# Kernel tuning notes

Measured on AMD Instinct MI355X. Metric: run time of the kernel, lower is better.

## Reference

```python
import jax, jax.numpy as jnp
from jax import lax
import numpy as np

TOP_K = 2
CAPACITY_FACTOR = 1.0


def setup_inputs() -> dict:
    key = jax.random.key(0)
    kx, kg, k1, k2 = jax.random.split(key, 4)
    B, S, D, F, E = 8, 4096, 512, 1024, 16
    x = jax.random.normal(kx, (B, S, D), dtype=jnp.float32)
    w_gate = jax.random.normal(kg, (D, E), dtype=jnp.float32) * 0.02
    w1 = jax.random.normal(k1, (E, D, 2 * F), dtype=jnp.float32) * 0.02
    w2 = jax.random.normal(k2, (E, F, D), dtype=jnp.float32) * 0.02
    return {"x": x, "w_gate": w_gate, "w1": w1, "w2": w2}


def reference(x, w_gate, w1, w2):
    # Inference mode: no gating noise, dropout is identity.
    B, S, D = x.shape
    E = w_gate.shape[1]
    T = B * S
    capacity = max(1, int(CAPACITY_FACTOR * T / E))  # static

    flat = x.reshape(T, D)
    gate_logits = flat @ w_gate                      # [T, E]
    gate_scores = jax.nn.softmax(gate_logits, axis=-1)
    topk_vals, topk_idx = lax.top_k(gate_scores, TOP_K)  # [T, k]

    phi_mean = gate_scores.mean(axis=0)
    aux_loss = E * jnp.sum(phi_mean * phi_mean)

    # Per-expert combine weight for every token: [E, T]
    onehot = topk_idx[None, :, :] == jnp.arange(E)[:, None, None]  # [E, T, k]
    w_et = jnp.sum(jnp.where(onehot, topk_vals[None], 0.0), axis=-1)  # [E, T]

    # Capacity truncation: keep the `capacity` highest-weight tokens per expert
    sel_w, sel_idx = lax.top_k(w_et, capacity)  # [E, C]; unrouted picks have weight 0

    xs = flat[sel_idx]                                  # [E, C, D] gather
    h = jnp.einsum('ecd,edf->ecf', xs, w1)              # [E, C, 2F]
    h1, h2 = jnp.split(h, 2, axis=-1)
    act = h1 * jax.nn.silu(h2)                          # SwiGLU
    out_e = jnp.einsum('ecf,efd->ecd', act, w2) * sel_w[..., None]  # [E, C, D]

    combined = jnp.zeros((T, D), dtype=flat.dtype).at[sel_idx.reshape(-1)].add(
        out_e.reshape(-1, D))
    return combined.reshape(B, S, D), aux_loss
```

## Files before the change

kernel.cpp:

```cpp
#include <hip/hip_runtime.h>
#include <hip/hip_bf16.h>
#include <math.h>

#define T_TOK 32768
#define D_DIM 512
#define E_EXP 16
#define F_DIM 1024
#define C_CAP 2048

typedef __attribute__((ext_vector_type(8))) __bf16 bf16x8;
typedef __attribute__((ext_vector_type(4))) float f32x4;

__device__ __forceinline__ unsigned short f2bf(float f) {
  unsigned u = __float_as_uint(f);
  u += 0x7FFFu + ((u >> 16) & 1u);
  return (unsigned short)(u >> 16);
}

__device__ __forceinline__ void gld16(const void* gptr, void* ldsptr) {
  __builtin_amdgcn_global_load_lds(
      (__attribute__((address_space(1))) void*)(void*)gptr,
      (__attribute__((address_space(3))) void*)ldsptr, 16, 0, 0);
}

__global__ void transpose_conv_kernel(const float* __restrict__ in,
                                      unsigned short* __restrict__ out,
                                      int R, int Cc) {
  __shared__ float tile[32][33];
  int e = blockIdx.z;
  int r0 = blockIdx.y * 32, c0 = blockIdx.x * 32;
  const float* pin = in + (size_t)e * R * Cc;
  unsigned short* pout = out + (size_t)e * R * Cc;
  int tx = threadIdx.x, ty = threadIdx.y;
  #pragma unroll
  for (int i = 0; i < 32; i += 8)
    tile[ty + i][tx] = pin[(size_t)(r0 + ty + i) * Cc + c0 + tx];
  __syncthreads();
  #pragma unroll
  for (int i = 0; i < 32; i += 8)
    pout[(size_t)(c0 + ty + i) * R + r0 + tx] = f2bf(tile[tx][ty + i]);
}

__global__ __launch_bounds__(256) void gate_kernel(
    const float* __restrict__ x, const float* __restrict__ wg,
    float* __restrict__ w_et, float* __restrict__ phi_sum,
    unsigned short* __restrict__ xb) {
  __shared__ float wgl[D_DIM * E_EXP];
  __shared__ float phil[E_EXP];
  int tid = threadIdx.x;
  for (int i = tid; i < D_DIM * E_EXP; i += 256) wgl[i] = wg[i];
  if (tid < E_EXP) phil[tid] = 0.f;
  __syncthreads();

  int g = tid >> 4;
  int e = tid & 15;
  int t = blockIdx.x * 16 + g;

  float acc = 0.f;
  const float* xr = x + (size_t)t * D_DIM;
  #pragma unroll 4
  for (int d = 0; d < D_DIM; d += 4) {
    float4 xv = *(const float4*)(xr + d);
    acc = fmaf(xv.x, wgl[(d + 0) * 16 + e], acc);
    acc = fmaf(xv.y, wgl[(d + 1) * 16 + e], acc);
    acc = fmaf(xv.z, wgl[(d + 2) * 16 + e], acc);
    acc = fmaf(xv.w, wgl[(d + 3) * 16 + e], acc);
  }

  unsigned short* xrow = xb + (size_t)t * D_DIM;
  #pragma unroll
  for (int j = 0; j < 8; ++j) {
    int idx = j * 16 + e;
    float4 v = *(const float4*)(xr + idx * 4);
    ushort4 o;
    o.x = f2bf(v.x); o.y = f2bf(v.y); o.z = f2bf(v.z); o.w = f2bf(v.w);
    ((ushort4*)xrow)[idx] = o;
  }

  float m = acc;
  for (int off = 8; off; off >>= 1) m = fmaxf(m, __shfl_xor(m, off));
  float p = expf(acc - m);
  float s = p;
  for (int off = 8; off; off >>= 1) s += __shfl_xor(s, off);
  float score = p / s;
  atomicAdd(&phil[e], score);

  float v1 = score; int i1 = e;
  for (int off = 8; off; off >>= 1) {
    float ov = __shfl_xor(v1, off); int oi = __shfl_xor(i1, off);
    if (ov > v1 || (ov == v1 && oi < i1)) { v1 = ov; i1 = oi; }
  }
  float sc2 = (e == i1) ? -1.f : score;
  float v2 = sc2; int i2 = e;
  for (int off = 8; off; off >>= 1) {
    float ov = __shfl_xor(v2, off); int oi = __shfl_xor(i2, off);
    if (ov > v2 || (ov == v2 && oi < i2)) { v2 = ov; i2 = oi; }
  }
  if (e == 0) {
    w_et[(size_t)i1 * T_TOK + t] = v1;
    w_et[(size_t)i2 * T_TOK + t] = v2;
  }
  __syncthreads();
  if (tid < E_EXP) atomicAdd(&phi_sum[tid], phil[tid]);
}

__global__ void aux_kernel(const float* __restrict__ phi_sum, float* __restrict__ out_aux) {
  if (threadIdx.x == 0) {
    float s = 0.f;
    for (int e = 0; e < E_EXP; ++e) {
      float pm = phi_sum[e] / (float)T_TOK;
      s += pm * pm;
    }
    *out_aux = (float)E_EXP * s;
  }
}

__global__ __launch_bounds__(1024) void select_kernel(
    const float* __restrict__ w_et, int* __restrict__ sel_idx, float* __restrict__ sel_w) {
  int e = blockIdx.x, tid = threadIdx.x;
  const float* w = w_et + (size_t)e * T_TOK;
  __shared__ unsigned hist[256];
  __shared__ unsigned scan_buf[1024];
  __shared__ unsigned sh_prefix, sh_k, sh_ngt, sh_cnt;

  unsigned prefix = 0, k = C_CAP, n_gt = 0;
  for (int pass = 0; pass < 4; ++pass) {
    int shift = 24 - pass * 8;
    if (tid < 256) hist[tid] = 0;
    if (tid == 0) sh_cnt = 0;
    __syncthreads();
    for (int i = tid; i < T_TOK; i += 1024) {
      unsigned b = __float_as_uint(w[i]);
      bool match = (pass == 0) || ((b >> (shift + 8)) == (prefix >> (shift + 8)));
      if (match) atomicAdd(&hist[(b >> shift) & 0xFFu], 1u);
    }
    __syncthreads();
    if (tid == 0) {
      unsigned cum = 0; int b = 255;
      for (; b > 0; --b) {
        unsigned c = hist[b];
        if (cum + c >= k) break;
        cum += c;
      }
      sh_prefix = prefix | ((unsigned)b << shift);
      sh_k = k - cum;
      sh_ngt = n_gt + cum;
    }
    __syncthreads();
    prefix = sh_prefix; k = sh_k; n_gt = sh_ngt;
    __syncthreads();
  }

  unsigned thr = prefix;
  unsigned eq_take = k;
  int base = tid * 32;

  unsigned myeq = 0;
  for (int i = base; i < base + 32; ++i) {
    float v = w[i];
    unsigned b = __float_as_uint(v);
    if (b > thr) {
      unsigned pos = atomicAdd(&sh_cnt, 1u);
      sel_idx[(size_t)e * C_CAP + pos] = i;
      sel_w[(size_t)e * C_CAP + pos] = v;
    } else if (b == thr) {
      myeq++;
    }
  }
  scan_buf[tid] = myeq;
  __syncthreads();
  for (int off = 1; off < 1024; off <<= 1) {
    unsigned add = (tid >= off) ? scan_buf[tid - off] : 0u;
    __syncthreads();
    scan_buf[tid] += add;
    __syncthreads();
  }
  unsigned excl = scan_buf[tid] - myeq;

  if (thr != 0u) {
    unsigned r = excl;
    for (int i = base; i < base + 32 && r < eq_take; ++i) {
      unsigned b = __float_as_uint(w[i]);
      if (b == thr) {
        sel_idx[(size_t)e * C_CAP + n_gt + r] = i;
        sel_w[(size_t)e * C_CAP + n_gt + r] = w[i];
        r++;
      }
    }
  }
  unsigned m_e = (thr != 0u) ? (unsigned)C_CAP : n_gt;
  for (unsigned i = m_e + tid; i < C_CAP; i += 1024) {
    sel_idx[(size_t)e * C_CAP + i] = 0;
    sel_w[(size_t)e * C_CAP + i] = 0.f;
  }
}

__global__ __launch_bounds__(256) void gemm1_kernel(
    const unsigned short* __restrict__ xb,
    const unsigned short* __restrict__ w1t,
    const int* __restrict__ sel_idx,
    unsigned short* __restrict__ act) {
  __shared__ __align__(16) unsigned short As[128 * 64];
  __shared__ __align__(16) unsigned short Bs[128 * 64];
  int bid = (blockIdx.x & 7) * 512 + (blockIdx.x >> 3);
  int nt = bid & 15, mt = (bid >> 4) & 15, e = bid >> 8;
  int tid = threadIdx.x, lane = tid & 63, wid = tid >> 6;

  const unsigned short* ag[4];
  const unsigned short* bg[4];
  unsigned lofs[4];
  #pragma unroll
  for (int s = 0; s < 4; ++s) {
    int c = s * 256 + tid;
    int row = c >> 3, kc = c & 7;
    int kcs = kc ^ (row & 7);
    int tok = sel_idx[e * C_CAP + mt * 128 + row];
    ag[s] = xb + (size_t)tok * D_DIM + kcs * 8;
    int hcol = (row < 64) ? (nt * 64 + row) : (F_DIM + nt * 64 + (row - 64));
    bg[s] = w1t + ((size_t)e * 2 * F_DIM + hcol) * D_DIM + kcs * 8;
    lofs[s] = (unsigned)(s * 256 + wid * 64) * 16;
  }

  f32x4 zero = {0.f, 0.f, 0.f, 0.f};
  f32x4 acc[2][8];
  #pragma unroll
  for (int m = 0; m < 2; ++m)
    #pragma unroll
    for (int n = 0; n < 8; ++n) acc[m][n] = zero;

  int cl = lane & 15, rg = lane >> 4;
  int sw = cl & 7;

  for (int kt = 0; kt < D_DIM / 64; ++kt) {
    #pragma unroll
    for (int s = 0; s < 4; ++s) {
      gld16(ag[s] + kt * 64, (char*)As + lofs[s]);
      gld16(bg[s] + kt * 64, (char*)Bs + lofs[s]);
    }
    __syncthreads();
    #pragma unroll
    for (int kk = 0; kk < 64; kk += 32) {
      int cofs = (((kk >> 3) + rg) ^ sw) << 3;
      bf16x8 a[2], b[8];
      #pragma unroll
      for (int m = 0; m < 2; ++m)
        a[m] = *(const bf16x8*)&As[(wid * 32 + m * 16 + cl) * 64 + cofs];
      #pragma unroll
      for (int n = 0; n < 8; ++n)
        b[n] = *(const bf16x8*)&Bs[(n * 16 + cl) * 64 + cofs];
      #pragma unroll
      for (int m = 0; m < 2; ++m)
        #pragma unroll
        for (int n = 0; n < 8; ++n)
          acc[m][n] = __builtin_amdgcn_mfma_f32_16x16x32_bf16(a[m], b[n], acc[m][n], 0, 0, 0);
    }
    __syncthreads();
  }

  #pragma unroll
  for (int m = 0; m < 2; ++m) {
    #pragma unroll
    for (int n = 0; n < 4; ++n) {
      #pragma unroll
      for (int r = 0; r < 4; ++r) {
        int row = mt * 128 + wid * 32 + m * 16 + rg * 4 + r;
        int col = nt * 64 + n * 16 + cl;
        float h1 = acc[m][n][r];
        float h2 = acc[m][n + 4][r];
        float sg = h2 / (1.f + __expf(-h2));
        act[((size_t)e * C_CAP + row) * F_DIM + col] = f2bf(h1 * sg);
      }
    }
  }
}

__global__ __launch_bounds__(256) void gemm2_kernel(
    const unsigned short* __restrict__ act,
    const unsigned short* __restrict__ w2t,
    const int* __restrict__ sel_idx,
    const float* __restrict__ sel_w,
    float* __restrict__ out) {
  __shared__ __align__(16) unsigned short As[128 * 64];
  __shared__ __align__(16) unsigned short Bs[128 * 64];
  int bid = (blockIdx.x & 7) * 128 + (blockIdx.x >> 3);
  int nt = bid & 3, mt = (bid >> 2) & 15, e = bid >> 6;
  int tid = threadIdx.x, lane = tid & 63, wid = tid >> 6;
  int wr = wid >> 1, wc = wid & 1;

  const unsigned short* ag[4];
  const unsigned short* bg[4];
  unsigned lofs[4];
  #pragma unroll
  for (int s = 0; s < 4; ++s) {
    int c = s * 256 + tid;
    int row = c >> 3, kc = c & 7;
    int kcs = kc ^ (row & 7);
    ag[s] = act + ((size_t)e * C_CAP + mt * 128 + row) * F_DIM + kcs * 8;
    int dcol = nt * 128 + row;
    bg[s] = w2t + ((size_t)e * D_DIM + dcol) * F_DIM + kcs * 8;
    lofs[s] = (unsigned)(s * 256 + wid * 64) * 16;
  }

  f32x4 zero = {0.f, 0.f, 0.f, 0.f};
  f32x4 acc[4][4];
  #pragma unroll
  for (int m = 0; m < 4; ++m)
    #pragma unroll
    for (int n = 0; n < 4; ++n) acc[m][n] = zero;

  int cl = lane & 15, rg = lane >> 4;
  int sw = cl & 7;

  for (int kt = 0; kt < F_DIM / 64; ++kt) {
    #pragma unroll
    for (int s = 0; s < 4; ++s) {
      gld16(ag[s] + kt * 64, (char*)As + lofs[s]);
      gld16(bg[s] + kt * 64, (char*)Bs + lofs[s]);
    }
    __syncthreads();
    #pragma unroll
    for (int kk = 0; kk < 64; kk += 32) {
      int cofs = (((kk >> 3) + rg) ^ sw) << 3;
      bf16x8 a[4], b[4];
      #pragma unroll
      for (int m = 0; m < 4; ++m)
        a[m] = *(const bf16x8*)&As[(wr * 64 + m * 16 + cl) * 64 + cofs];
      #pragma unroll
      for (int n = 0; n < 4; ++n)
        b[n] = *(const bf16x8*)&Bs[(wc * 64 + n * 16 + cl) * 64 + cofs];
      #pragma unroll
      for (int m = 0; m < 4; ++m)
        #pragma unroll
        for (int n = 0; n < 4; ++n)
          acc[m][n] = __builtin_amdgcn_mfma_f32_16x16x32_bf16(a[m], b[n], acc[m][n], 0, 0, 0);
    }
    __syncthreads();
  }

  #pragma unroll
  for (int m = 0; m < 4; ++m) {
    #pragma unroll
    for (int r = 0; r < 4; ++r) {
      int slot = mt * 128 + wr * 64 + m * 16 + rg * 4 + r;
      float wgt = sel_w[e * C_CAP + slot];
      int tok = sel_idx[e * C_CAP + slot];
      float* orow = out + (size_t)tok * D_DIM;
      #pragma unroll
      for (int n = 0; n < 4; ++n) {
        int col = nt * 128 + wc * 64 + n * 16 + cl;
        atomicAdd(&orow[col], acc[m][n][r] * wgt);
      }
    }
  }
}

extern "C" void kernel_launch(void* const* d_in, const int* in_sizes, int n_in,
                              void* d_out, int out_size, void* d_ws, size_t ws_size,
                              hipStream_t stream) {
  const float* x  = (const float*)d_in[0];
  const float* wg = (const float*)d_in[1];
  const float* w1 = (const float*)d_in[2];
  const float* w2 = (const float*)d_in[3];
  float* out = (float*)d_out;

  char* ws = (char*)d_ws;
  size_t off = 0;
  auto carve = [&](size_t bytes) -> void* {
    void* p = ws + off;
    off += (bytes + 255) & ~(size_t)255;
    return p;
  };
  float* w_et            = (float*)carve((size_t)E_EXP * T_TOK * 4);
  float* phi             = (float*)carve(64);
  int* sel_i             = (int*)carve((size_t)E_EXP * C_CAP * 4);
  float* sel_wv          = (float*)carve((size_t)E_EXP * C_CAP * 4);
  unsigned short* xb     = (unsigned short*)carve((size_t)T_TOK * D_DIM * 2);
  unsigned short* w1t    = (unsigned short*)carve((size_t)E_EXP * 2 * F_DIM * D_DIM * 2);
  unsigned short* w2t    = (unsigned short*)carve((size_t)E_EXP * D_DIM * F_DIM * 2);
  unsigned short* actb   = (unsigned short*)carve((size_t)E_EXP * C_CAP * F_DIM * 2);
  if (off > ws_size) return;

  hipMemsetAsync(w_et, 0, (size_t)E_EXP * T_TOK * 4, stream);
  hipMemsetAsync(phi, 0, 64, stream);
  hipMemsetAsync(d_out, 0, (size_t)out_size * 4, stream);

  transpose_conv_kernel<<<dim3(2 * F_DIM / 32, D_DIM / 32, E_EXP), dim3(32, 8), 0, stream>>>(
      w1, w1t, D_DIM, 2 * F_DIM);
  transpose_conv_kernel<<<dim3(D_DIM / 32, F_DIM / 32, E_EXP), dim3(32, 8), 0, stream>>>(
      w2, w2t, F_DIM, D_DIM);
  gate_kernel<<<T_TOK / 16, 256, 0, stream>>>(x, wg, w_et, phi, xb);
  select_kernel<<<E_EXP, 1024, 0, stream>>>(w_et, sel_i, sel_wv);
  aux_kernel<<<1, 64, 0, stream>>>(phi, out + (size_t)T_TOK * D_DIM);
  gemm1_kernel<<<E_EXP * 16 * 16, 256, 0, stream>>>(xb, w1t, sel_i, actb);
  gemm2_kernel<<<E_EXP * 16 * 4, 256, 0, stream>>>(actb, w2t, sel_i, sel_wv, out);
}
```

Baseline: 410.6 us.

## Parallelize capacity top-k selection and triple-buffer both expert GEMMs

The single-block-per-expert radix select is replaced by a multi-kernel, grid-parallel radix select over 11/11/10-bit digits, followed by count, prefix-base and write phases spread across 256 blocks. Both GEMM kernels move to a BK=32, three-stage LDS pipeline using async global-to-LDS loads with explicit vmcnt waits, plus a new swizzle and a 2x2 wave tiling for gemm1. The aim is to remove the serial bottleneck of 16 blocks scanning 32K elements and to hide global load latency in the GEMMs. The cost is more kernel launches and extra histogram buffers that must be zeroed, and the select path now handles the case of fewer than capacity nonzero weights differently.

Result: faster. 336.4 us (-18.1%).

```diff
diff --git a/kernel.cpp b/kernel.cpp
--- a/kernel.cpp
+++ b/kernel.cpp
@@ -115,191 +115,283 @@
   }
 }
 
-__global__ __launch_bounds__(1024) void select_kernel(
-    const float* __restrict__ w_et, int* __restrict__ sel_idx, float* __restrict__ sel_w) {
-  int e = blockIdx.x, tid = threadIdx.x;
-  const float* w = w_et + (size_t)e * T_TOK;
-  __shared__ unsigned hist[256];
-  __shared__ unsigned scan_buf[1024];
-  __shared__ unsigned sh_prefix, sh_k, sh_ngt, sh_cnt;
-
-  unsigned prefix = 0, k = C_CAP, n_gt = 0;
-  for (int pass = 0; pass < 4; ++pass) {
-    int shift = 24 - pass * 8;
-    if (tid < 256) hist[tid] = 0;
-    if (tid == 0) sh_cnt = 0;
+template<int P>
+__global__ __launch_bounds__(256) void s_hist(
+    const float* __restrict__ w_et, unsigned* __restrict__ hist,
+    const unsigned* __restrict__ prefix, const unsigned* __restrict__ done) {
+  int c = blockIdx.x, e = blockIdx.y, tid = threadIdx.x;
+  if (P > 0 && done[e]) return;
+  __shared__ unsigned lh[2048];
+  for (int i = tid; i < 2048; i += 256) lh[i] = 0;
+  __syncthreads();
+  const float* w = w_et + (size_t)e * T_TOK + c * 2048;
+  unsigned pfx = (P > 0) ? prefix[e] : 0u;
+  #pragma unroll
+  for (int i = 0; i < 8; ++i) {
+    unsigned b = __float_as_uint(w[i * 256 + tid]);
+    if (P == 0) { if (b) atomicAdd(&lh[b >> 21], 1u); }
+    else if (P == 1) { if ((b >> 21) == (pfx >> 21)) atomicAdd(&lh[(b >> 10) & 0x7FFu], 1u); }
+    else { if ((b >> 10) == (pfx >> 10)) atomicAdd(&lh[b & 0x3FFu], 1u); }
+  }
+  __syncthreads();
+  for (int i = tid; i < 2048; i += 256)
+    if (lh[i]) atomicAdd(&hist[e * 2048 + i], lh[i]);
+}
+
+template<int P>
+__global__ __launch_bounds__(1024) void s_pick(
+    const unsigned* __restrict__ hist, unsigned* __restrict__ prefix,
+    unsigned* __restrict__ krem, unsigned* __restrict__ done) {
+  int tid = threadIdx.x, lane = tid & 63, e = tid >> 6;
+  if (P > 0 && done[e]) return;
+  const int BPL = (P == 2) ? 16 : 32;
+  const int SH = (P == 0) ? 21 : (P == 1) ? 10 : 0;
+  const unsigned* h = hist + e * 2048;
+  unsigned S = 0;
+  for (int i = 0; i < BPL; ++i) S += h[lane * BPL + i];
+  unsigned U = S;
+  #pragma unroll
+  for (int off = 1; off < 64; off <<= 1) {
+    unsigned t = __shfl_down(U, off);
+    if (lane + off < 64) U += t;
+  }
+  unsigned Unext = __shfl_down(U, 1);
+  if (lane == 63) Unext = 0;
+  unsigned k = (P == 0) ? (unsigned)C_CAP : krem[e];
+  if (P == 0 && lane == 0) {
+    if (U < k) { done[e] = 1; prefix[e] = 0; krem[e] = 0; }
+    else done[e] = 0;
+  }
+  if (U >= k && Unext < k) {
+    unsigned cum = Unext; int chosen = 0; unsigned knew = 0;
+    for (int i = BPL - 1; i >= 0; --i) {
+      unsigned hh = h[lane * BPL + i];
+      if (cum + hh >= k) { chosen = lane * BPL + i; knew = k - cum; break; }
+      cum += hh;
+    }
+    if (P == 0) prefix[e] = ((unsigned)chosen) << SH;
+    else prefix[e] = prefix[e] | (((unsigned)chosen) << SH);
+    krem[e] = knew;
+  }
+}
+
+__global__ __launch_bounds__(256) void s_count(
+    const float* __restrict__ w_et, const unsigned* __restrict__ prefix,
+    unsigned* __restrict__ cnt) {
+  int c = blockIdx.x, e = blockIdx.y, tid = threadIdx.x;
+  unsigned thr = prefix[e];
+  const uint4* up = (const uint4*)(w_et + (size_t)e * T_TOK + c * 2048 + tid * 8);
+  uint4 va = up[0], vb = up[1];
+  unsigned gt = 0, eq = 0;
+  unsigned vals[8] = {va.x, va.y, va.z, va.w, vb.x, vb.y, vb.z, vb.w};
+  #pragma unroll
+  for (int i = 0; i < 8; ++i) {
+    if (vals[i] > thr) gt++;
+    else if (vals[i] == thr) eq++;
+  }
+  __shared__ unsigned sc[256];
+  sc[tid] = (gt << 16) | eq;
+  __syncthreads();
+  for (int s = 128; s; s >>= 1) {
+    if (tid < s) sc[tid] += sc[tid + s];
     __syncthreads();
-    for (int i = tid; i < T_TOK; i += 1024) {
-      unsigned b = __float_as_uint(w[i]);
-      bool match = (pass == 0) || ((b >> (shift + 8)) == (prefix >> (shift + 8)));
-      if (match) atomicAdd(&hist[(b >> shift) & 0xFFu], 1u);
+  }
+  if (tid == 0) cnt[e * 16 + c] = sc[0];
+}
+
+__global__ __launch_bounds__(64) void s_base(
+    const unsigned* __restrict__ cnt, unsigned* __restrict__ gbase,
+    unsigned* __restrict__ ebase, unsigned* __restrict__ gtt,
+    unsigned* __restrict__ eqt) {
+  int e = threadIdx.x;
+  if (e >= 16) return;
+  unsigned g = 0, q = 0;
+  #pragma unroll
+  for (int c = 0; c < 16; ++c) {
+    unsigned p = cnt[e * 16 + c];
+    gbase[e * 16 + c] = g;
+    ebase[e * 16 + c] = q;
+    g += p >> 16;
+    q += p & 0xFFFFu;
+  }
+  gtt[e] = g;
+  eqt[e] = (unsigned)C_CAP - g;
+}
+
+__global__ __launch_bounds__(256) void s_write(
+    const float* __restrict__ w_et, const unsigned* __restrict__ prefix,
+    const unsigned* __restrict__ gbase, const unsigned* __restrict__ ebase,
+    const unsigned* __restrict__ gtt, const unsigned* __restrict__ eqt,
+    int* __restrict__ sel_idx, float* __restrict__ sel_w) {
+  int c = blockIdx.x, e = blockIdx.y, tid = threadIdx.x;
+  unsigned thr = prefix[e];
+  const uint4* up = (const uint4*)(w_et + (size_t)e * T_TOK + c * 2048 + tid * 8);
+  uint4 va = up[0], vb = up[1];
+  unsigned vals[8] = {va.x, va.y, va.z, va.w, vb.x, vb.y, vb.z, vb.w};
+  unsigned gt = 0, eq = 0;
+  #pragma unroll
+  for (int i = 0; i < 8; ++i) {
+    if (vals[i] > thr) gt++;
+    else if (vals[i] == thr) eq++;
+  }
+  __shared__ unsigned sc[256];
+  unsigned mine = (gt << 16) | eq;
+  sc[tid] = mine;
+  __syncthreads();
+  for (int off = 1; off < 256; off <<= 1) {
+    unsigned add = (tid >= off) ? sc[tid - off] : 0u;
+    __syncthreads();
+    sc[tid] += add;
+    __syncthreads();
+  }
+  unsigned excl = sc[tid] - mine;
+  unsigned gpos = gbase[e * 16 + c] + (excl >> 16);
+  unsigned qpos = ebase[e * 16 + c] + (excl & 0xFFFFu);
+  unsigned gtotal = gtt[e], eqtake = eqt[e];
+  int* si = sel_idx + (size_t)e * C_CAP;
+  float* sw = sel_w + (size_t)e * C_CAP;
+  int tokbase = c * 2048 + tid * 8;
+  #pragma unroll
+  for (int i = 0; i < 8; ++i) {
+    unsigned b = vals[i];
+    if (b > thr) {
+      si[gpos] = tokbase + i; sw[gpos] = __uint_as_float(b); gpos++;
+    } else if (b == thr && qpos < eqtake) {
+      si[gtotal + qpos] = tokbase + i; sw[gtotal + qpos] = __uint_as_float(b); qpos++;
     }
-    __syncthreads();
-    if (tid == 0) {
-      unsigned cum = 0; int b = 255;
-      for (; b > 0; --b) {
-        unsigned c = hist[b];
-        if (cum + c >= k) break;
-        cum += c;
-      }
-      sh_prefix = prefix | ((unsigned)b << shift);
-      sh_k = k - cum;
-      sh_ngt = n_gt + cum;
-    }
-    __syncthreads();
-    prefix = sh_prefix; k = sh_k; n_gt = sh_ngt;
-    __syncthreads();
-  }
-
-  unsigned thr = prefix;
-  unsigned eq_take = k;
-  int base = tid * 32;
-
-  unsigned myeq = 0;
-  for (int i = base; i < base + 32; ++i) {
-    float v = w[i];
-    unsigned b = __float_as_uint(v);
-    if (b > thr) {
-      unsigned pos = atomicAdd(&sh_cnt, 1u);
-      sel_idx[(size_t)e * C_CAP + pos] = i;
-      sel_w[(size_t)e * C_CAP + pos] = v;
-    } else if (b == thr) {
-      myeq++;
-    }
-  }
-  scan_buf[tid] = myeq;
-  __syncthreads();
-  for (int off = 1; off < 1024; off <<= 1) {
-    unsigned add = (tid >= off) ? scan_buf[tid - off] : 0u;
-    __syncthreads();
-    scan_buf[tid] += add;
-    __syncthreads();
-  }
-  unsigned excl = scan_buf[tid] - myeq;
-
-  if (thr != 0u) {
-    unsigned r = excl;
-    for (int i = base; i < base + 32 && r < eq_take; ++i) {
-      unsigned b = __float_as_uint(w[i]);
-      if (b == thr) {
-        sel_idx[(size_t)e * C_CAP + n_gt + r] = i;
-        sel_w[(size_t)e * C_CAP + n_gt + r] = w[i];
-        r++;
-      }
-    }
-  }
-  unsigned m_e = (thr != 0u) ? (unsigned)C_CAP : n_gt;
-  for (unsigned i = m_e + tid; i < C_CAP; i += 1024) {
-    sel_idx[(size_t)e * C_CAP + i] = 0;
-    sel_w[(size_t)e * C_CAP + i] = 0.f;
-  }
-}
-
-__global__ __launch_bounds__(256) void gemm1_kernel(
+  }
+}
+
+
+#define PIPE_BARRIER() do { __builtin_amdgcn_s_barrier(); __builtin_amdgcn_sched_barrier(0); } while (0)
+
+__global__ __launch_bounds__(256, 3) void gemm1_kernel(
     const unsigned short* __restrict__ xb,
     const unsigned short* __restrict__ w1t,
     const int* __restrict__ sel_idx,
     unsigned short* __restrict__ act) {
-  __shared__ __align__(16) unsigned short As[128 * 64];
-  __shared__ __align__(16) unsigned short Bs[128 * 64];
+  __shared__ __align__(16) unsigned short As[3 * 4096];
+  __shared__ __align__(16) unsigned short Bs[3 * 4096];
   int bid = (blockIdx.x & 7) * 512 + (blockIdx.x >> 3);
   int nt = bid & 15, mt = (bid >> 4) & 15, e = bid >> 8;
   int tid = threadIdx.x, lane = tid & 63, wid = tid >> 6;
-
-  const unsigned short* ag[4];
-  const unsigned short* bg[4];
-  unsigned lofs[4];
-  #pragma unroll
-  for (int s = 0; s < 4; ++s) {
-    int c = s * 256 + tid;
-    int row = c >> 3, kc = c & 7;
-    int kcs = kc ^ (row & 7);
-    int tok = sel_idx[e * C_CAP + mt * 128 + row];
-    ag[s] = xb + (size_t)tok * D_DIM + kcs * 8;
-    int hcol = (row < 64) ? (nt * 64 + row) : (F_DIM + nt * 64 + (row - 64));
-    bg[s] = w1t + ((size_t)e * 2 * F_DIM + hcol) * D_DIM + kcs * 8;
-    lofs[s] = (unsigned)(s * 256 + wid * 64) * 16;
-  }
+  int wr = wid >> 1, wc = wid & 1;
+  int cl = lane & 15, rg = lane >> 4;
+
+  int c0 = tid, c1 = 256 + tid;
+  int r0 = c0 >> 2, gk0 = (c0 & 3) ^ ((r0 >> 1) & 3);
+  int r1 = c1 >> 2, gk1 = (c1 & 3) ^ ((r1 >> 1) & 3);
+  int tok0 = sel_idx[e * C_CAP + mt * 128 + r0];
+  int tok1 = sel_idx[e * C_CAP + mt * 128 + r1];
+  const unsigned short* ag0 = xb + (size_t)tok0 * D_DIM + gk0 * 8;
+  const unsigned short* ag1 = xb + (size_t)tok1 * D_DIM + gk1 * 8;
+  int hcol0 = (r0 < 64) ? (nt * 64 + r0) : (F_DIM + nt * 64 + (r0 - 64));
+  int hcol1 = (r1 < 64) ? (nt * 64 + r1) : (F_DIM + nt * 64 + (r1 - 64));
+  const unsigned short* bg0 = w1t + ((size_t)e * 2 * F_DIM + hcol0) * D_DIM + gk0 * 8;
+  const unsigned short* bg1 = w1t + ((size_t)e * 2 * F_DIM + hcol1) * D_DIM + gk1 * 8;
+  char* Ab = (char*)As;
+  char* Bb = (char*)Bs;
+
+#define G1_STAGE(buf, kt) do { \
+    gld16(ag0 + (kt) * 32, Ab + (buf) * 8192 + tid * 16); \
+    gld16(ag1 + (kt) * 32, Ab + (buf) * 8192 + 4096 + tid * 16); \
+    gld16(bg0 + (kt) * 32, Bb + (buf) * 8192 + tid * 16); \
+    gld16(bg1 + (kt) * 32, Bb + (buf) * 8192 + 4096 + tid * 16); \
+  } while (0)
 
   f32x4 zero = {0.f, 0.f, 0.f, 0.f};
-  f32x4 acc[2][8];
-  #pragma unroll
-  for (int m = 0; m < 2; ++m)
+  f32x4 acc[4][4];
+  #pragma unroll
+  for (int m = 0; m < 4; ++m)
     #pragma unroll
-    for (int n = 0; n < 8; ++n) acc[m][n] = zero;
-
-  int cl = lane & 15, rg = lane >> 4;
-  int sw = cl & 7;
-
-  for (int kt = 0; kt < D_DIM / 64; ++kt) {
+    for (int n = 0; n < 4; ++n) acc[m][n] = zero;
+
+#define G1_COMPUTE(buf) do { \
+    const unsigned short* Ap = As + (buf) * 4096; \
+    const unsigned short* Bp = Bs + (buf) * 4096; \
+    bf16x8 av[4], bv[4]; \
+    _Pragma("unroll") \
+    for (int m = 0; m < 4; ++m) { \
+      int ra = wr * 64 + m * 16 + cl; \
+      av[m] = *(const bf16x8*)&Ap[(ra * 4 + (rg ^ ((ra >> 1) & 3))) * 8]; \
+    } \
+    _Pragma("unroll") \
+    for (int n = 0; n < 4; ++n) { \
+      int rb = ((n < 2) ? (wc * 32 + n * 16) : (64 + wc * 32 + (n - 2) * 16)) + cl; \
+      bv[n] = *(const bf16x8*)&Bp[(rb * 4 + (rg ^ ((rb >> 1) & 3))) * 8]; \
+    } \
+    _Pragma("unroll") \
+    for (int m = 0; m < 4; ++m) \
+      _Pragma("unroll") \
+      for (int n = 0; n < 4; ++n) \
+        acc[m][n] = __builtin_amdgcn_mfma_f32_16x16x32_bf16(av[m], bv[n], acc[m][n], 0, 0, 0); \
+  } while (0)
+
+  const int NK = D_DIM / 32;
+  G1_STAGE(0, 0);
+  G1_STAGE(1, 1);
+  int bc = 0, bs = 2;
+  for (int kt = 0; kt < NK - 1; ++kt) {
+    asm volatile("s_waitcnt vmcnt(4)" ::: "memory");
+    PIPE_BARRIER();
+    if (kt + 2 < NK) { G1_STAGE(bs, kt + 2); bs = (bs == 2) ? 0 : bs + 1; }
+    __builtin_amdgcn_sched_barrier(0);
+    G1_COMPUTE(bc);
+    bc = (bc == 2) ? 0 : bc + 1;
+  }
+  asm volatile("s_waitcnt vmcnt(0)" ::: "memory");
+  PIPE_BARRIER();
+  G1_COMPUTE(bc);
+
+  #pragma unroll
+  for (int m = 0; m < 4; ++m) {
     #pragma unroll
-    for (int s = 0; s < 4; ++s) {
-      gld16(ag[s] + kt * 64, (char*)As + lofs[s]);
-      gld16(bg[s] + kt * 64, (char*)Bs + lofs[s]);
-    }
-    __syncthreads();
-    #pragma unroll
-    for (int kk = 0; kk < 64; kk += 32) {
-      int cofs = (((kk >> 3) + rg) ^ sw) << 3;
-      bf16x8 a[2], b[8];
-      #pragma unroll
-      for (int m = 0; m < 2; ++m)
-        a[m] = *(const bf16x8*)&As[(wid * 32 + m * 16 + cl) * 64 + cofs];
-      #pragma unroll
-      for (int n = 0; n < 8; ++n)
-        b[n] = *(const bf16x8*)&Bs[(n * 16 + cl) * 64 + cofs];
-      #pragma unroll
-      for (int m = 0; m < 2; ++m)
-        #pragma unroll
-        for (int n = 0; n < 8; ++n)
-          acc[m][n] = __builtin_amdgcn_mfma_f32_16x16x32_bf16(a[m], b[n], acc[m][n], 0, 0, 0);
-    }
-    __syncthreads();
-  }
-
-  #pragma unroll
-  for (int m = 0; m < 2; ++m) {
-    #pragma unroll
-    for (int n = 0; n < 4; ++n) {
+    for (int n = 0; n < 2; ++n) {
       #pragma unroll
       for (int r = 0; r < 4; ++r) {
-        int row = mt * 128 + wid * 32 + m * 16 + rg * 4 + r;
-        int col = nt * 64 + n * 16 + cl;
+        int row = mt * 128 + wr * 64 + m * 16 + rg * 4 + r;
+        int col = nt * 64 + wc * 32 + n * 16 + cl;
         float h1 = acc[m][n][r];
-        float h2 = acc[m][n + 4][r];
+        float h2 = acc[m][n + 2][r];
         float sg = h2 / (1.f + __expf(-h2));
         act[((size_t)e * C_CAP + row) * F_DIM + col] = f2bf(h1 * sg);
       }
     }
   }
-}
-
-__global__ __launch_bounds__(256) void gemm2_kernel(
+#undef G1_STAGE
+#undef G1_COMPUTE
+}
+
+__global__ __launch_bounds__(256, 3) void gemm2_kernel(
     const unsigned short* __restrict__ act,
     const unsigned short* __restrict__ w2t,
     const int* __restrict__ sel_idx,
     const float* __restrict__ sel_w,
     float* __restrict__ out) {
-  __shared__ __align__(16) unsigned short As[128 * 64];
-  __shared__ __align__(16) unsigned short Bs[128 * 64];
+  __shared__ __align__(16) unsigned short As[3 * 4096];
+  __shared__ __align__(16) unsigned short Bs[3 * 4096];
   int bid = (blockIdx.x & 7) * 128 + (blockIdx.x >> 3);
   int nt = bid & 3, mt = (bid >> 2) & 15, e = bid >> 6;
   int tid = threadIdx.x, lane = tid & 63, wid = tid >> 6;
   int wr = wid >> 1, wc = wid & 1;
-
-  const unsigned short* ag[4];
-  const unsigned short* bg[4];
-  unsigned lofs[4];
-  #pragma unroll
-  for (int s = 0; s < 4; ++s) {
-    int c = s * 256 + tid;
-    int row = c >> 3, kc = c & 7;
-    int kcs = kc ^ (row & 7);
-    ag[s] = act + ((size_t)e * C_CAP + mt * 128 + row) * F_DIM + kcs * 8;
-    int dcol = nt * 128 + row;
-    bg[s] = w2t + ((size_t)e * D_DIM + dcol) * F_DIM + kcs * 8;
-    lofs[s] = (unsigned)(s * 256 + wid * 64) * 16;
-  }
+  int cl = lane & 15, rg = lane >> 4;
+
+  int c0 = tid, c1 = 256 + tid;
+  int r0 = c0 >> 2, gk0 = (c0 & 3) ^ ((r0 >> 1) & 3);
+  int r1 = c1 >> 2, gk1 = (c1 & 3) ^ ((r1 >> 1) & 3);
+  const unsigned short* ag0 = act + ((size_t)e * C_CAP + mt * 128 + r0) * F_DIM + gk0 * 8;
+  const unsigned short* ag1 = act + ((size_t)e * C_CAP + mt * 128 + r1) * F_DIM + gk1 * 8;
+  const unsigned short* bg0 = w2t + ((size_t)e * D_DIM + nt * 128 + r0) * F_DIM + gk0 * 8;
+  const unsigned short* bg1 = w2t + ((size_t)e * D_DIM + nt * 128 + r1) * F_DIM + gk1 * 8;
+  char* Ab = (char*)As;
+  char* Bb = (char*)Bs;
+
+#define G2_STAGE(buf, kt) do { \
+    gld16(ag0 + (kt) * 32, Ab + (buf) * 8192 + tid * 16); \
+    gld16(ag1 + (kt) * 32, Ab + (buf) * 8192 + 4096 + tid * 16); \
+    gld16(bg0 + (kt) * 32, Bb + (buf) * 8192 + tid * 16); \
+    gld16(bg1 + (kt) * 32, Bb + (buf) * 8192 + 4096 + tid * 16); \
+  } while (0)
 
   f32x4 zero = {0.f, 0.f, 0.f, 0.f};
   f32x4 acc[4][4];
@@ -308,34 +400,42 @@
     #pragma unroll
     for (int n = 0; n < 4; ++n) acc[m][n] = zero;
 
-  int cl = lane & 15, rg = lane >> 4;
-  int sw = cl & 7;
-
-  for (int kt = 0; kt < F_DIM / 64; ++kt) {
-    #pragma unroll
-    for (int s = 0; s < 4; ++s) {
-      gld16(ag[s] + kt * 64, (char*)As + lofs[s]);
-      gld16(bg[s] + kt * 64, (char*)Bs + lofs[s]);
-    }
-    __syncthreads();
-    #pragma unroll
-    for (int kk = 0; kk < 64; kk += 32) {
-      int cofs = (((kk >> 3) + rg) ^ sw) << 3;
-      bf16x8 a[4], b[4];
-      #pragma unroll
-      for (int m = 0; m < 4; ++m)
-        a[m] = *(const bf16x8*)&As[(wr * 64 + m * 16 + cl) * 64 + cofs];
-      #pragma unroll
-      for (int n = 0; n < 4; ++n)
-        b[n] = *(const bf16x8*)&Bs[(wc * 64 + n * 16 + cl) * 64 + cofs];
-      #pragma unroll
-      for (int m = 0; m < 4; ++m)
-        #pragma unroll
-        for (int n = 0; n < 4; ++n)
-          acc[m][n] = __builtin_amdgcn_mfma_f32_16x16x32_bf16(a[m], b[n], acc[m][n], 0, 0, 0);
-    }
-    __syncthreads();
-  }
+#define G2_COMPUTE(buf) do { \
+    const unsigned short* Ap = As + (buf) * 4096; \
+    const unsigned short* Bp = Bs + (buf) * 4096; \
+    bf16x8 av[4], bv[4]; \
+    _Pragma("unroll") \
+    for (int m = 0; m < 4; ++m) { \
+      int ra = wr * 64 + m * 16 + cl; \
+      av[m] = *(const bf16x8*)&Ap[(ra * 4 + (rg ^ ((ra >> 1) & 3))) * 8]; \
+    } \
+    _Pragma("unroll") \
+    for (int n = 0; n < 4; ++n) { \
+      int rb = wc * 64 + n * 16 + cl; \
+      bv[n] = *(const bf16x8*)&Bp[(rb * 4 + (rg ^ ((rb >> 1) & 3))) * 8]; \
+    } \
+    _Pragma("unroll") \
+    for (int m = 0; m < 4; ++m) \
+      _Pragma("unroll") \
+      for (int n = 0; n < 4; ++n) \
+        acc[m][n] = __builtin_amdgcn_mfma_f32_16x16x32_bf16(av[m], bv[n], acc[m][n], 0, 0, 0); \
+  } while (0)
+
+  const int NK = F_DIM / 32;
+  G2_STAGE(0, 0);
+  G2_STAGE(1, 1);
+  int bc = 0, bs = 2;
+  for (int kt = 0; kt < NK - 1; ++kt) {
+    asm volatile("s_waitcnt vmcnt(4)" ::: "memory");
+    PIPE_BARRIER();
+    if (kt + 2 < NK) { G2_STAGE(bs, kt + 2); bs = (bs == 2) ? 0 : bs + 1; }
+    __builtin_amdgcn_sched_barrier(0);
+    G2_COMPUTE(bc);
+    bc = (bc == 2) ? 0 : bc + 1;
+  }
+  asm volatile("s_waitcnt vmcnt(0)" ::: "memory");
+  PIPE_BARRIER();
+  G2_COMPUTE(bc);
 
   #pragma unroll
   for (int m = 0; m < 4; ++m) {
@@ -352,6 +452,8 @@
       }
     }
   }
+#undef G2_STAGE
+#undef G2_COMPUTE
 }
 
 extern "C" void kernel_launch(void* const* d_in, const int* in_sizes, int n_in,
@@ -378,10 +480,22 @@
   unsigned short* w1t    = (unsigned short*)carve((size_t)E_EXP * 2 * F_DIM * D_DIM * 2);
   unsigned short* w2t    = (unsigned short*)carve((size_t)E_EXP * D_DIM * F_DIM * 2);
   unsigned short* actb   = (unsigned short*)carve((size_t)E_EXP * C_CAP * F_DIM * 2);
+  unsigned* hist0        = (unsigned*)carve((size_t)E_EXP * 2048 * 4);
+  unsigned* hist1        = (unsigned*)carve((size_t)E_EXP * 2048 * 4);
+  unsigned* hist2        = (unsigned*)carve((size_t)E_EXP * 2048 * 4);
+  unsigned* prefix       = (unsigned*)carve(64 * 4);
+  unsigned* krem         = (unsigned*)carve(64 * 4);
+  unsigned* done         = (unsigned*)carve(64 * 4);
+  unsigned* cnt          = (unsigned*)carve(256 * 4);
+  unsigned* gbase        = (unsigned*)carve(256 * 4);
+  unsigned* ebase        = (unsigned*)carve(256 * 4);
+  unsigned* gtt          = (unsigned*)carve(64 * 4);
+  unsigned* eqt          = (unsigned*)carve(64 * 4);
   if (off > ws_size) return;
 
   hipMemsetAsync(w_et, 0, (size_t)E_EXP * T_TOK * 4, stream);
   hipMemsetAsync(phi, 0, 64, stream);
+  hipMemsetAsync(hist0, 0, (size_t)E_EXP * 2048 * 4 * 3, stream);
   hipMemsetAsync(d_out, 0, (size_t)out_size * 4, stream);
 
   transpose_conv_kernel<<<dim3(2 * F_DIM / 32, D_DIM / 32, E_EXP), dim3(32, 8), 0, stream>>>(
@@ -389,7 +503,18 @@
   transpose_conv_kernel<<<dim3(D_DIM / 32, F_DIM / 32, E_EXP), dim3(32, 8), 0, stream>>>(
       w2, w2t, F_DIM, D_DIM);
   gate_kernel<<<T_TOK / 16, 256, 0, stream>>>(x, wg, w_et, phi, xb);
-  select_kernel<<<E_EXP, 1024, 0, stream>>>(w_et, sel_i, sel_wv);
+
+  s_hist<0><<<dim3(16, 16), 256, 0, stream>>>(w_et, hist0, prefix, done);
+  s_pick<0><<<1, 1024, 0, stream>>>(hist0, prefix, krem, done);
+  s_hist<1><<<dim3(16, 16), 256, 0, stream>>>(w_et, hist1, prefix, done);
+  s_pick<1><<<1, 1024, 0, stream>>>(hist1, prefix, krem, done);
+  s_hist<2><<<dim3(16, 16), 256, 0, stream>>>(w_et, hist2, prefix, done);
+  s_pick<2><<<1, 1024, 0, stream>>>(hist2, prefix, krem, done);
+  s_count<<<dim3(16, 16), 256, 0, stream>>>(w_et, prefix, cnt);
+  s_base<<<1, 64, 0, stream>>>(cnt, gbase, ebase, gtt, eqt);
+  s_write<<<dim3(16, 16), 256, 0, stream>>>(w_et, prefix, gbase, ebase, gtt, eqt,
+                                            sel_i, sel_wv);
+
   aux_kernel<<<1, 64, 0, stream>>>(phi, out + (size_t)T_TOK * D_DIM);
   gemm1_kernel<<<E_EXP * 16 * 16, 256, 0, stream>>>(xb, w1t, sel_i, actb);
   gemm2_kernel<<<E_EXP * 16 * 4, 256, 0, stream>>>(actb, w2t, sel_i, sel_wv, out);
```
